# Optimization experiments

Hardware: AMD Instinct MI355X
Metric: run time of the kernel (lower is better)

The kernel has to match this reference:

```python
import jax, jax.numpy as jnp
import numpy as np

LN_EPS = 1e-5


def setup_inputs() -> dict:
    key = jax.random.key(0)
    k1, k2, k3 = jax.random.split(key, 3)
    N, E, D_IN, D_OUT = 50000, 500000, 128, 128
    x = jax.random.normal(k1, (N, D_IN), dtype=jnp.float32)
    edge_index = jax.random.randint(k2, (2, E), 0, N, dtype=jnp.int64)
    W = jax.random.normal(k3, (D_IN, D_OUT), dtype=jnp.float32) * (1.0 / np.sqrt(D_IN))
    b = jnp.zeros((D_OUT,), dtype=jnp.float32)
    ln_gamma = jnp.ones((D_OUT,), dtype=jnp.float32)
    ln_beta = jnp.zeros((D_OUT,), dtype=jnp.float32)
    return {"x": x, "edge_index": edge_index, "W": W, "b": b,
            "ln_gamma": ln_gamma, "ln_beta": ln_beta}


def reference(x, edge_index, W, b, ln_gamma, ln_beta):
    N = x.shape[0]
    # GCNConv: linear transform first (no fused bias; bias added after aggregation)
    h = x @ W  # [N, D_out]
    # add self-loops
    loops = jnp.arange(N, dtype=edge_index.dtype)
    src = jnp.concatenate([edge_index[0], loops])  # [E+N]
    dst = jnp.concatenate([edge_index[1], loops])  # [E+N]
    # symmetric normalization deg^{-1/2} (degree computed on dst, incl. self-loops)
    deg = jax.ops.segment_sum(jnp.ones(src.shape, dtype=h.dtype), dst, num_segments=N)
    dinv = jnp.where(deg > 0, jax.lax.rsqrt(deg), 0.0)
    norm = dinv[src] * dinv[dst]  # [E+N]
    # gather messages, scale, scatter-add to destinations
    msgs = h[src] * norm[:, None]  # [E+N, D_out]
    out = jax.ops.segment_sum(msgs, dst, num_segments=N) + b  # [N, D_out]
    # LayerNorm over features
    mu = out.mean(axis=-1, keepdims=True)
    var = out.var(axis=-1, keepdims=True)
    out = (out - mu) * jax.lax.rsqrt(var + LN_EPS) * ln_gamma + ln_beta
    # activation
    return jax.nn.relu(out)
```

## Files before the change

### kernel.cpp

```cpp
#include <hip/hip_runtime.h>
#include <hip/hip_fp16.h>
#include <math.h>

#define D 128
#define LN_EPS 1e-5f
#define BKT 64
#define EPT 8

typedef _Float16 f16x8 __attribute__((ext_vector_type(8)));
typedef float    f32x4 __attribute__((ext_vector_type(4)));

__global__ void prep_kernel(const float* __restrict__ W, _Float16* __restrict__ wtg,
                            int* __restrict__ degi, int N) {
    int idx = blockIdx.x * 256 + threadIdx.x;
    int k = idx >> 7;
    int n = idx & 127;
    wtg[n * D + k] = (_Float16)W[k * D + n];
    for (int i = idx; i < N; i += 64 * 256) degi[i] = 0;
}

__global__ void gemm_kernel(const float* __restrict__ x, const _Float16* __restrict__ wtg,
                            unsigned* __restrict__ h2, int N) {
    __shared__ _Float16 xs[64][136];
    int tid = threadIdx.x;

    int row0 = blockIdx.x * 64;
#pragma unroll
    for (int i = 0; i < 8; ++i) {
        int idx = i * 256 + tid;
        int r   = idx >> 5;
        int c4  = idx & 31;
        float4 v = make_float4(0.f, 0.f, 0.f, 0.f);
        if (row0 + r < N) v = *(const float4*)&x[(size_t)(row0 + r) * D + c4 * 4];
        __half2 lo = __floats2half2_rn(v.x, v.y);
        __half2 hi = __floats2half2_rn(v.z, v.w);
        *(__half2*)&xs[r][c4 * 4]     = lo;
        *(__half2*)&xs[r][c4 * 4 + 2] = hi;
    }
    __syncthreads();

    int l     = tid & 63;
    int mtile = tid >> 6;
    int mn    = l & 15;
    int kq    = (l >> 4) * 8;
    f32x4 acc[8];
#pragma unroll
    for (int nt = 0; nt < 8; ++nt) acc[nt] = (f32x4){0.f, 0.f, 0.f, 0.f};

#pragma unroll
    for (int ks = 0; ks < 4; ++ks) {
        int kb = ks * 32 + kq;
        f16x8 a = *(f16x8*)&xs[mtile * 16 + mn][kb];
#pragma unroll
        for (int nt = 0; nt < 8; ++nt) {
            f16x8 bf = *(const f16x8*)&wtg[(nt * 16 + mn) * D + kb];
            acc[nt] = __builtin_amdgcn_mfma_f32_16x16x32_f16(a, bf, acc[nt], 0, 0, 0);
        }
    }

    int quad = l >> 4;
#pragma unroll
    for (int nt = 0; nt < 8; ++nt) {
#pragma unroll
        for (int rg = 0; rg < 4; ++rg) {
            float v  = acc[nt][rg];
            float pv = __shfl_xor(v, 1);
            if (!(l & 1)) {
                int row = row0 + mtile * 16 + quad * 4 + rg;
                if (row < N) {
                    __half2 p = __floats2half2_rn(v, pv);
                    h2[(size_t)row * (D / 2) + nt * 8 + (mn >> 1)] = *(unsigned*)&p;
                }
            }
        }
    }
}

__global__ void bucket_kernel(const int* __restrict__ src, const int* __restrict__ dst,
                              int* __restrict__ degi, int* __restrict__ bucket, int E) {
    int t  = blockIdx.x * 256 + threadIdx.x;
    int e0 = t * EPT;
    if (e0 >= E) return;
    if (e0 + EPT <= E) {
        int4 da = *(const int4*)&dst[e0];
        int4 db = *(const int4*)&dst[e0 + 4];
        int4 sa = *(const int4*)&src[e0];
        int4 sb = *(const int4*)&src[e0 + 4];
        int d[8] = {da.x, da.y, da.z, da.w, db.x, db.y, db.z, db.w};
        int s[8] = {sa.x, sa.y, sa.z, sa.w, sb.x, sb.y, sb.z, sb.w};
        int p[8];
#pragma unroll
        for (int j = 0; j < 8; ++j) p[j] = atomicAdd(&degi[d[j]], 1);
#pragma unroll
        for (int j = 0; j < 8; ++j)
            if (p[j] < BKT) bucket[(size_t)d[j] * BKT + p[j]] = s[j];
    } else {
        for (int e = e0; e < E; ++e) {
            int d = dst[e];
            int p = atomicAdd(&degi[d], 1);
            if (p < BKT) bucket[(size_t)d * BKT + p] = src[e];
        }
    }
}

__device__ __forceinline__ void acc_edge(float& a0, float& a1, unsigned u, float w) {
    __half2 hv = *(__half2*)&u;
    a0 = fmaf(__low2float(hv),  w, a0);
    a1 = fmaf(__high2float(hv), w, a1);
}

__global__ void gather_ln_kernel(const int* __restrict__ bucket, const int* __restrict__ degi,
                                 const unsigned* __restrict__ h2, const float* __restrict__ b,
                                 const float* __restrict__ g, const float* __restrict__ be,
                                 float* __restrict__ out, int N) {
    int row  = blockIdx.x * 4 + (threadIdx.x >> 6);
    int lane = threadIdx.x & 63;
    if (row >= N) return;
    int dg   = degi[row];
    int dgc  = dg < BKT ? dg : BKT;
    float di = rsqrtf((float)dg + 1.0f);
    float sw = di * di;
    unsigned su = h2[(size_t)row * (D / 2) + lane];
    float acc0 = 0.f, acc1 = 0.f;
    acc_edge(acc0, acc1, su, sw);
    const int* bk = bucket + (size_t)row * BKT;

    int e = 0;
    for (; e + 8 <= dgc; e += 8) {
        int4 ra = *(const int4*)&bk[e];
        int4 rb = *(const int4*)&bk[e + 4];
        int s[8] = {ra.x, ra.y, ra.z, ra.w, rb.x, rb.y, rb.z, rb.w};
        unsigned u[8]; float wgt[8];
#pragma unroll
        for (int j = 0; j < 8; ++j) u[j] = h2[(size_t)s[j] * (D / 2) + lane];
#pragma unroll
        for (int j = 0; j < 8; ++j) wgt[j] = rsqrtf((float)degi[s[j]] + 1.0f) * di;
#pragma unroll
        for (int j = 0; j < 8; ++j) acc_edge(acc0, acc1, u[j], wgt[j]);
    }
    int rem = dgc - e;
    if (rem & 4) {
        int4 ra = *(const int4*)&bk[e];
        int s[4] = {ra.x, ra.y, ra.z, ra.w};
        unsigned u[4]; float wgt[4];
#pragma unroll
        for (int j = 0; j < 4; ++j) u[j] = h2[(size_t)s[j] * (D / 2) + lane];
#pragma unroll
        for (int j = 0; j < 4; ++j) wgt[j] = rsqrtf((float)degi[s[j]] + 1.0f) * di;
#pragma unroll
        for (int j = 0; j < 4; ++j) acc_edge(acc0, acc1, u[j], wgt[j]);
        e += 4;
    }
    if (rem & 2) {
        int s0 = bk[e], s1 = bk[e + 1];
        unsigned u0 = h2[(size_t)s0 * (D / 2) + lane];
        unsigned u1 = h2[(size_t)s1 * (D / 2) + lane];
        float w0 = rsqrtf((float)degi[s0] + 1.0f) * di;
        float w1 = rsqrtf((float)degi[s1] + 1.0f) * di;
        acc_edge(acc0, acc1, u0, w0);
        acc_edge(acc0, acc1, u1, w1);
        e += 2;
    }
    if (rem & 1) {
        int s0 = bk[e];
        unsigned u0 = h2[(size_t)s0 * (D / 2) + lane];
        float w0 = rsqrtf((float)degi[s0] + 1.0f) * di;
        acc_edge(acc0, acc1, u0, w0);
    }

    float2 bb = *(const float2*)&b[lane * 2];
    float v0 = acc0 + bb.x;
    float v1 = acc1 + bb.y;
    float s = v0 + v1;
    float q = v0 * v0 + v1 * v1;
#pragma unroll
    for (int off = 32; off; off >>= 1) {
        s += __shfl_xor(s, off);
        q += __shfl_xor(q, off);
    }
    float mean = s * (1.0f / 128.0f);
    float var  = q * (1.0f / 128.0f) - mean * mean;
    float rstd = rsqrtf(var + LN_EPS);
    float2 gg = *(const float2*)&g[lane * 2];
    float2 eb = *(const float2*)&be[lane * 2];
    float y0 = (v0 - mean) * rstd * gg.x + eb.x;
    float y1 = (v1 - mean) * rstd * gg.y + eb.y;
    *(float2*)&out[(size_t)row * D + lane * 2] = make_float2(fmaxf(y0, 0.0f), fmaxf(y1, 0.0f));
}

extern "C" void kernel_launch(void* const* d_in, const int* in_sizes, int n_in,
                              void* d_out, int out_size, void* d_ws, size_t ws_size,
                              hipStream_t stream) {
    const float* x  = (const float*)d_in[0];
    const int*   ei = (const int*)d_in[1];
    const float* W  = (const float*)d_in[2];
    const float* b  = (const float*)d_in[3];
    const float* g  = (const float*)d_in[4];
    const float* be = (const float*)d_in[5];

    int N = in_sizes[0] / D;
    int E = in_sizes[1] / 2;
    const int* src = ei;
    const int* dst = ei + E;

    float* out = (float*)d_out;

    char* w = (char*)d_ws;
    unsigned* h2    = (unsigned*)w;           w += (size_t)N * (D / 2) * sizeof(unsigned);
    int*      degi  = (int*)w;                w += (size_t)N * sizeof(int);
    _Float16* wtg   = (_Float16*)w;           w += (size_t)D * D * sizeof(_Float16);
    int*      bucket= (int*)w;                w += (size_t)N * BKT * sizeof(int);

    int nbG = (N + 63) / 64;
    int nbB = (E + 256 * EPT - 1) / (256 * EPT);

    prep_kernel  <<<64,  256, 0, stream>>>(W, wtg, degi, N);
    gemm_kernel  <<<nbG, 256, 0, stream>>>(x, wtg, h2, N);
    bucket_kernel<<<nbB, 256, 0, stream>>>(src, dst, degi, bucket, E);
    gather_ln_kernel<<<(N + 3) / 4, 256, 0, stream>>>(bucket, degi, h2,
                                                      b, g, be, out, N);
}
```

Baseline: 158.5 us.

## Fuse GEMM and edge bucketing into one launch; pad degree counters

Merges the GEMM and edge-bucketing kernels into a single launch, with extra blocks handling the edges so both run concurrently and one launch is removed. The degree counter array is padded to one counter per 64 bytes, so atomics to different nodes do not contend on the same cache line. The cost is a larger degree array (N*16 ints) to zero in prep, and scattered, uncoalesced degree reads in the gather kernel.

Result: no change. 158.0 us (-0.3%).

```diff
diff --git a/kernel.cpp b/kernel.cpp
--- a/kernel.cpp
+++ b/kernel.cpp
@@ -6,6 +6,7 @@
 #define LN_EPS 1e-5f
 #define BKT 64
 #define EPT 8
+#define DPAD 16
 
 typedef _Float16 f16x8 __attribute__((ext_vector_type(8)));
 typedef float    f32x4 __attribute__((ext_vector_type(4)));
@@ -16,13 +17,44 @@
     int k = idx >> 7;
     int n = idx & 127;
     wtg[n * D + k] = (_Float16)W[k * D + n];
-    for (int i = idx; i < N; i += 64 * 256) degi[i] = 0;
-}
-
-__global__ void gemm_kernel(const float* __restrict__ x, const _Float16* __restrict__ wtg,
-                            unsigned* __restrict__ h2, int N) {
+    int4 z = make_int4(0, 0, 0, 0);
+    int nq = N * (DPAD / 4);
+    for (int i = idx; i < nq; i += 64 * 256) ((int4*)degi)[i] = z;
+}
+
+__global__ void fused_kernel(const float* __restrict__ x, const _Float16* __restrict__ wtg,
+                             unsigned* __restrict__ h2,
+                             const int* __restrict__ src, const int* __restrict__ dst,
+                             int* __restrict__ degi, int* __restrict__ bucket,
+                             int N, int E, int nbG) {
     __shared__ _Float16 xs[64][136];
     int tid = threadIdx.x;
+
+    if ((int)blockIdx.x >= nbG) {
+        int e0 = ((blockIdx.x - nbG) * 256 + tid) * EPT;
+        if (e0 >= E) return;
+        if (e0 + EPT <= E) {
+            int4 da = *(const int4*)&dst[e0];
+            int4 db = *(const int4*)&dst[e0 + 4];
+            int4 sa = *(const int4*)&src[e0];
+            int4 sb = *(const int4*)&src[e0 + 4];
+            int d[8] = {da.x, da.y, da.z, da.w, db.x, db.y, db.z, db.w};
+            int s[8] = {sa.x, sa.y, sa.z, sa.w, sb.x, sb.y, sb.z, sb.w};
+            int p[8];
+#pragma unroll
+            for (int j = 0; j < 8; ++j) p[j] = atomicAdd(&degi[(size_t)d[j] * DPAD], 1);
+#pragma unroll
+            for (int j = 0; j < 8; ++j)
+                if (p[j] < BKT) bucket[(size_t)d[j] * BKT + p[j]] = s[j];
+        } else {
+            for (int e = e0; e < E; ++e) {
+                int d = dst[e];
+                int p = atomicAdd(&degi[(size_t)d * DPAD], 1);
+                if (p < BKT) bucket[(size_t)d * BKT + p] = src[e];
+            }
+        }
+        return;
+    }
 
     int row0 = blockIdx.x * 64;
 #pragma unroll
@@ -76,33 +108,6 @@
     }
 }
 
-__global__ void bucket_kernel(const int* __restrict__ src, const int* __restrict__ dst,
-                              int* __restrict__ degi, int* __restrict__ bucket, int E) {
-    int t  = blockIdx.x * 256 + threadIdx.x;
-    int e0 = t * EPT;
-    if (e0 >= E) return;
-    if (e0 + EPT <= E) {
-        int4 da = *(const int4*)&dst[e0];
-        int4 db = *(const int4*)&dst[e0 + 4];
-        int4 sa = *(const int4*)&src[e0];
-        int4 sb = *(const int4*)&src[e0 + 4];
-        int d[8] = {da.x, da.y, da.z, da.w, db.x, db.y, db.z, db.w};
-        int s[8] = {sa.x, sa.y, sa.z, sa.w, sb.x, sb.y, sb.z, sb.w};
-        int p[8];
-#pragma unroll
-        for (int j = 0; j < 8; ++j) p[j] = atomicAdd(&degi[d[j]], 1);
-#pragma unroll
-        for (int j = 0; j < 8; ++j)
-            if (p[j] < BKT) bucket[(size_t)d[j] * BKT + p[j]] = s[j];
-    } else {
-        for (int e = e0; e < E; ++e) {
-            int d = dst[e];
-            int p = atomicAdd(&degi[d], 1);
-            if (p < BKT) bucket[(size_t)d * BKT + p] = src[e];
-        }
-    }
-}
-
 __device__ __forceinline__ void acc_edge(float& a0, float& a1, unsigned u, float w) {
     __half2 hv = *(__half2*)&u;
     a0 = fmaf(__low2float(hv),  w, a0);
@@ -116,7 +121,7 @@
     int row  = blockIdx.x * 4 + (threadIdx.x >> 6);
     int lane = threadIdx.x & 63;
     if (row >= N) return;
-    int dg   = degi[row];
+    int dg   = degi[(size_t)row * DPAD];
     int dgc  = dg < BKT ? dg : BKT;
     float di = rsqrtf((float)dg + 1.0f);
     float sw = di * di;
@@ -134,7 +139,7 @@
 #pragma unroll
         for (int j = 0; j < 8; ++j) u[j] = h2[(size_t)s[j] * (D / 2) + lane];
 #pragma unroll
-        for (int j = 0; j < 8; ++j) wgt[j] = rsqrtf((float)degi[s[j]] + 1.0f) * di;
+        for (int j = 0; j < 8; ++j) wgt[j] = rsqrtf((float)degi[(size_t)s[j] * DPAD] + 1.0f) * di;
 #pragma unroll
         for (int j = 0; j < 8; ++j) acc_edge(acc0, acc1, u[j], wgt[j]);
     }
@@ -146,7 +151,7 @@
 #pragma unroll
         for (int j = 0; j < 4; ++j) u[j] = h2[(size_t)s[j] * (D / 2) + lane];
 #pragma unroll
-        for (int j = 0; j < 4; ++j) wgt[j] = rsqrtf((float)degi[s[j]] + 1.0f) * di;
+        for (int j = 0; j < 4; ++j) wgt[j] = rsqrtf((float)degi[(size_t)s[j] * DPAD] + 1.0f) * di;
 #pragma unroll
         for (int j = 0; j < 4; ++j) acc_edge(acc0, acc1, u[j], wgt[j]);
         e += 4;
@@ -155,8 +160,8 @@
         int s0 = bk[e], s1 = bk[e + 1];
         unsigned u0 = h2[(size_t)s0 * (D / 2) + lane];
         unsigned u1 = h2[(size_t)s1 * (D / 2) + lane];
-        float w0 = rsqrtf((float)degi[s0] + 1.0f) * di;
-        float w1 = rsqrtf((float)degi[s1] + 1.0f) * di;
+        float w0 = rsqrtf((float)degi[(size_t)s0 * DPAD] + 1.0f) * di;
+        float w1 = rsqrtf((float)degi[(size_t)s1 * DPAD] + 1.0f) * di;
         acc_edge(acc0, acc1, u0, w0);
         acc_edge(acc0, acc1, u1, w1);
         e += 2;
@@ -164,7 +169,7 @@
     if (rem & 1) {
         int s0 = bk[e];
         unsigned u0 = h2[(size_t)s0 * (D / 2) + lane];
-        float w0 = rsqrtf((float)degi[s0] + 1.0f) * di;
+        float w0 = rsqrtf((float)degi[(size_t)s0 * DPAD] + 1.0f) * di;
         acc_edge(acc0, acc1, u0, w0);
     }
 
@@ -207,16 +212,16 @@
 
     char* w = (char*)d_ws;
     unsigned* h2    = (unsigned*)w;           w += (size_t)N * (D / 2) * sizeof(unsigned);
-    int*      degi  = (int*)w;                w += (size_t)N * sizeof(int);
+    int*      degi  = (int*)w;                w += (size_t)N * DPAD * sizeof(int);
     _Float16* wtg   = (_Float16*)w;           w += (size_t)D * D * sizeof(_Float16);
     int*      bucket= (int*)w;                w += (size_t)N * BKT * sizeof(int);
 
     int nbG = (N + 63) / 64;
     int nbB = (E + 256 * EPT - 1) / (256 * EPT);
 
-    prep_kernel  <<<64,  256, 0, stream>>>(W, wtg, degi, N);
-    gemm_kernel  <<<nbG, 256, 0, stream>>>(x, wtg, h2, N);
-    bucket_kernel<<<nbB, 256, 0, stream>>>(src, dst, degi, bucket, E);
+    prep_kernel <<<64,        256, 0, stream>>>(W, wtg, degi, N);
+    fused_kernel<<<nbG + nbB, 256, 0, stream>>>(x, wtg, h2, src, dst, degi, bucket,
+                                                N, E, nbG);
     gather_ln_kernel<<<(N + 3) / 4, 256, 0, stream>>>(bucket, degi, h2,
                                                       b, g, be, out, N);
 }
```
